# Kernel tuning notes

Measured on AMD Instinct MI355X. Metric: run time of the kernel, lower is better.

Reference implementation:

```python
import jax, jax.numpy as jnp
import numpy as np

N_H = 16
N_KV = 4
D_K = 128
ROPE_BASE = 10000.0


def _rope(t, cos, sin):
    # t: [B, T, H, d_k]; cos/sin: [1, T, 1, d_k//2]
    te, to = t[..., 0::2], t[..., 1::2]
    oe = te * cos - to * sin
    oo = te * sin + to * cos
    return jnp.stack([oe, oo], axis=-1).reshape(t.shape)


def setup_inputs() -> dict:
    key = jax.random.key(0)
    ks = jax.random.split(key, 5)
    B, T, d = 4, 2048, 2048
    s = 0.02
    return {
        "x": jax.random.normal(ks[0], (B, T, d), jnp.float32),
        "Wq": jax.random.normal(ks[1], (d, d), jnp.float32) * s,
        "Wk": jax.random.normal(ks[2], (d, N_KV * D_K), jnp.float32) * s,
        "Wv": jax.random.normal(ks[3], (d, N_KV * D_K), jnp.float32) * s,
        "Wp": jax.random.normal(ks[4], (d, d), jnp.float32) * s,
        "bp": jnp.zeros((d,), jnp.float32),
    }


def reference(x, Wq, Wk, Wv, Wp, bp):
    B, T, C = x.shape
    g = N_H // N_KV  # group size

    q = (x @ Wq).reshape(B, T, N_H, D_K)
    k = (x @ Wk).reshape(B, T, N_KV, D_K)
    v = (x @ Wv).reshape(B, T, N_KV, D_K)

    # RoPE frequencies (constants)
    theta = ROPE_BASE ** (-2.0 * jnp.arange(0, D_K, 2, dtype=jnp.float32) / D_K)
    freq = jnp.arange(T, dtype=jnp.float32)[:, None] * theta[None, :]  # [T, d_k//2]
    cos = jnp.cos(freq)[None, :, None, :]
    sin = jnp.sin(freq)[None, :, None, :]
    q = _rope(q, cos, sin)
    k = _rope(k, cos, sin)

    # GQA: group q heads by shared kv head (equiv to repeat_interleave on kv)
    q = q.reshape(B, T, N_KV, g, D_K).transpose(0, 2, 3, 1, 4)  # [B,n_kv,g,T,d_k]
    k = k.transpose(0, 2, 1, 3)  # [B,n_kv,T,d_k]
    v = v.transpose(0, 2, 1, 3)

    scores = jnp.einsum('bngqd,bnkd->bngqk', q, k) * (D_K ** -0.5)
    causal = jnp.tril(jnp.ones((T, T), bool))
    scores = jnp.where(causal, scores, -jnp.inf)
    attn = jax.nn.softmax(scores, axis=-1)
    out = jnp.einsum('bngqk,bnkd->bngqd', attn, v)  # [B,n_kv,g,T,d_k]
    out = out.transpose(0, 3, 1, 2, 4).reshape(B, T, C)
    return out @ Wp + bp
```

## Files before the change

### kernel.cpp

```cpp
#include <hip/hip_runtime.h>
#include <hip/hip_bf16.h>
#include <math.h>

typedef __bf16 bf16_t;
typedef __bf16 bf16x8 __attribute__((ext_vector_type(8)));
typedef __bf16 bf16x4 __attribute__((ext_vector_type(4)));
typedef float f32x4 __attribute__((ext_vector_type(4)));
typedef float f32x16 __attribute__((ext_vector_type(16)));
typedef unsigned int u32;

#define MFMA16 __builtin_amdgcn_mfma_f32_16x16x32_bf16
#define MFMA32 __builtin_amdgcn_mfma_f32_32x32x16_bf16

static __device__ __forceinline__ u32 pkbf(float a, float b) {
  union { bf16_t h[2]; u32 u; } z;
  z.h[0] = (bf16_t)a; z.h[1] = (bf16_t)b;
  return z.u;
}

static __device__ __forceinline__ void gload16(const bf16_t* g, bf16_t* l) {
  __builtin_amdgcn_global_load_lds(
      (const __attribute__((address_space(1))) void*)g,
      (__attribute__((address_space(3))) void*)l, 16, 0, 0);
}

__global__ void k_f32_to_bf16(const float* __restrict__ in, bf16_t* __restrict__ out, long n) {
  long i = ((long)blockIdx.x * blockDim.x + threadIdx.x) * 4;
  long stride = (long)gridDim.x * blockDim.x * 4;
  for (; i < n; i += stride) {
    const float4 v = *(const float4*)(in + i);
    bf16x4 o; o[0] = (bf16_t)v.x; o[1] = (bf16_t)v.y; o[2] = (bf16_t)v.z; o[3] = (bf16_t)v.w;
    *(bf16x4*)(out + i) = o;
  }
}

__global__ void k_transpose_bf16(const float* __restrict__ W, bf16_t* __restrict__ WT,
                                 int K, int N) {
  __shared__ float tile[32][33];
  int n0 = blockIdx.x * 32, k0 = blockIdx.y * 32;
  int tx = threadIdx.x & 31, ty = threadIdx.x >> 5;
#pragma unroll
  for (int i = 0; i < 4; i++)
    tile[ty + i * 8][tx] = W[(size_t)(k0 + ty + i * 8) * N + n0 + tx];
  __syncthreads();
#pragma unroll
  for (int i = 0; i < 4; i++) {
    int n = ty + i * 8;
    WT[(size_t)(n0 + n) * K + k0 + tx] = (bf16_t)tile[tx][n];
  }
}

__global__ void k_build_vt(const bf16_t* __restrict__ qkv, bf16_t* __restrict__ VT) {
  __shared__ bf16_t tile[32][33];
  int t0 = blockIdx.x * 32, c0 = blockIdx.y * 32, b = blockIdx.z;
  int tx = threadIdx.x & 31, ty = threadIdx.x >> 5;
  const bf16_t* src = qkv + (size_t)b * 2048 * 3072 + 2560;
#pragma unroll
  for (int i = 0; i < 4; i++)
    tile[ty + i * 8][tx] = src[(size_t)(t0 + ty + i * 8) * 3072 + c0 + tx];
  __syncthreads();
  bf16_t* dst = VT + (size_t)b * 512 * 2048;
#pragma unroll
  for (int i = 0; i < 4; i++)
    dst[(size_t)(c0 + ty + i * 8) * 2048 + t0 + tx] = tile[tx][ty + i * 8];
}

__global__ void k_rope(bf16_t* __restrict__ qkv) {
  int idx = blockIdx.x * blockDim.x + threadIdx.x;
  if (idx >= 8192 * 1280) return;
  int r = idx / 1280, p = idx - r * 1280;
  int t = r & 2047;
  int i = p & 63;
  float theta = exp2f(-(float)i * 0.41524101186092029f);
  float f = (float)t * theta;
  float s, c;
  sincosf(f, &s, &c);
  bf16_t* a = qkv + (size_t)r * 3072 + p * 2;
  float e = (float)a[0], o = (float)a[1];
  a[0] = (bf16_t)(e * c - o * s);
  a[1] = (bf16_t)(e * s + o * c);
}

template <bool F32OUT>
__global__ __launch_bounds__(512, 2) void k_gemm_bt(
    const bf16_t* __restrict__ A, const bf16_t* __restrict__ BT,
    bf16_t* __restrict__ Cb, float* __restrict__ Cf,
    const float* __restrict__ bias, int M, int N, int K, int nwg) {
  __shared__ bf16_t smem[65536];
  const int nbn = N >> 8;
  int orig = (int)blockIdx.x;
  int swz = (orig & 7) * (nwg >> 3) + (orig >> 3);
  int bm = swz / nbn, bn = swz % nbn;
  const int tid = threadIdx.x;
  const int lane = tid & 63, wid = tid >> 6;
  const int wm = (wid >> 2) << 7;
  const int wn = (wid & 3) << 6;
  const int lr = lane & 15, lq = lane >> 4;
  f32x4 acc[8][4] = {};

  const int rl = tid >> 3;
  const int ss = (tid & 7) ^ (rl & 7);
  const bf16_t* gA = A + (size_t)(bm * 256 + rl) * K + ss * 8;
  const bf16_t* gB = BT + (size_t)(bn * 256 + rl) * K + ss * 8;
  const int lo = wid * 512;

  const int nt = K >> 6;
  {
    bf16_t* sA0 = smem;
    bf16_t* sB0 = smem + 16384;
#pragma unroll
    for (int i = 0; i < 4; i++) {
      gload16(gA + (size_t)i * 64 * K, sA0 + i * 4096 + lo);
      gload16(gB + (size_t)i * 64 * K, sB0 + i * 4096 + lo);
    }
  }
  asm volatile("s_waitcnt vmcnt(0)" ::: "memory");
  __syncthreads();

  for (int t = 0; t < nt; ++t) {
    bf16_t* sAc = smem + (t & 1) * 32768;
    bf16_t* sBc = sAc + 16384;
    bf16_t* sAn = smem + ((t & 1) ^ 1) * 32768;
    bf16_t* sBn = sAn + 16384;
    const int k1 = (t + 1) << 6;
    bf16x8 breg[4][2];
#pragma unroll
    for (int n = 0; n < 4; n++)
#pragma unroll
      for (int kk = 0; kk < 2; kk++) {
        int R = wn + n * 16 + lr;
        int u = (kk * 4 + lq) ^ (R & 7);
        breg[n][kk] = *(const bf16x8*)&sBc[R * 64 + u * 8];
      }
    {
      bf16x8 areg[2][2];
#pragma unroll
      for (int ml = 0; ml < 2; ml++)
#pragma unroll
        for (int kk = 0; kk < 2; kk++) {
          int R = wm + ml * 16 + lr;
          int u = (kk * 4 + lq) ^ (R & 7);
          areg[ml][kk] = *(const bf16x8*)&sAc[R * 64 + u * 8];
        }
      if (t + 1 < nt) {
#pragma unroll
        for (int i = 0; i < 4; i++) {
          gload16(gA + (size_t)i * 64 * K + k1, sAn + i * 4096 + lo);
          gload16(gB + (size_t)i * 64 * K + k1, sBn + i * 4096 + lo);
        }
      }
      __builtin_amdgcn_s_barrier();
      asm volatile("s_waitcnt lgkmcnt(0)" ::: "memory");
      __builtin_amdgcn_sched_barrier(0);
      __builtin_amdgcn_s_setprio(1);
#pragma unroll
      for (int ml = 0; ml < 2; ml++)
#pragma unroll
        for (int n = 0; n < 4; n++)
#pragma unroll
          for (int kk = 0; kk < 2; kk++)
            acc[ml][n] = MFMA16(areg[ml][kk], breg[n][kk], acc[ml][n], 0, 0, 0);
      __builtin_amdgcn_s_setprio(0);
      __builtin_amdgcn_s_barrier();
    }
#pragma unroll
    for (int p = 1; p < 4; p++) {
      bf16x8 areg[2][2];
#pragma unroll
      for (int ml = 0; ml < 2; ml++)
#pragma unroll
        for (int kk = 0; kk < 2; kk++) {
          int R = wm + (2 * p + ml) * 16 + lr;
          int u = (kk * 4 + lq) ^ (R & 7);
          areg[ml][kk] = *(const bf16x8*)&sAc[R * 64 + u * 8];
        }
      __builtin_amdgcn_s_barrier();
      asm volatile("s_waitcnt lgkmcnt(0)" ::: "memory");
      __builtin_amdgcn_sched_barrier(0);
      __builtin_amdgcn_s_setprio(1);
#pragma unroll
      for (int ml = 0; ml < 2; ml++)
#pragma unroll
        for (int n = 0; n < 4; n++)
#pragma unroll
          for (int kk = 0; kk < 2; kk++)
            acc[2 * p + ml][n] = MFMA16(areg[ml][kk], breg[n][kk], acc[2 * p + ml][n], 0, 0, 0);
      __builtin_amdgcn_s_setprio(0);
      if (p == 3) {
        asm volatile("s_waitcnt vmcnt(0)" ::: "memory");
        __builtin_amdgcn_sched_barrier(0);
      }
      __builtin_amdgcn_s_barrier();
    }
  }
#pragma unroll
  for (int m = 0; m < 8; m++) {
    int row0 = bm * 256 + wm + m * 16 + lq * 4;
#pragma unroll
    for (int n = 0; n < 4; n++) {
      int col = bn * 256 + wn + n * 16 + lr;
#pragma unroll
      for (int r = 0; r < 4; r++) {
        if constexpr (F32OUT)
          Cf[(size_t)(row0 + r) * N + col] = acc[m][n][r] + bias[col];
        else
          Cb[(size_t)(row0 + r) * N + col] = (bf16_t)acc[m][n][r];
      }
    }
  }
}

__global__ __launch_bounds__(256, 2) void k_attn(const bf16_t* __restrict__ qkv,
                                                 const bf16_t* __restrict__ VT,
                                                 bf16_t* __restrict__ out) {
  __shared__ bf16_t sK[64 * 128];
  __shared__ bf16_t sVT[128 * 72];
  int bid = blockIdx.x;
  int g = bid >> 6;
  int qt = (g & 1) ? (g >> 1) : (15 - (g >> 1));
  int bh = bid & 63;
  int h = bh & 15, b = bh >> 4;
  int kvh = h >> 2;
  const size_t RS = 3072;
  const bf16_t* Qb = qkv + (size_t)b * 2048 * RS + h * 128;
  const bf16_t* Kb = qkv + (size_t)b * 2048 * RS + 2048 + kvh * 128;
  const bf16_t* Vt = VT + (size_t)(b * 4 + kvh) * 128 * 2048;
  int q0 = qt * 128;
  int tid = threadIdx.x, lane = tid & 63, wid = tid >> 6;
  int l31 = lane & 31, hi = lane >> 5;
  int qw = q0 + wid * 32;

  bf16x8 qf[8];
  {
    const bf16_t* qrow = Qb + (size_t)(qw + l31) * RS + hi * 8;
#pragma unroll
    for (int dc = 0; dc < 8; dc++)
      qf[dc] = *(const bf16x8*)(qrow + dc * 16);
  }

  f32x16 oT[4] = {};
  float m_r = -INFINITY, l_r = 0.f;
  const float SC = 0.08838834764831845f * 1.4426950408889634f;

  int k_row = tid >> 4, k_seg = tid & 15;
  int vd = tid >> 3, vk = (tid & 7) * 8;

  bf16x8 kreg[4], vreg[4];
  auto issue = [&](int k0) {
#pragma unroll
    for (int ps = 0; ps < 4; ps++)
      kreg[ps] = *(const bf16x8*)(Kb + (size_t)(k0 + k_row + ps * 16) * RS + k_seg * 8);
#pragma unroll
    for (int ps = 0; ps < 4; ps++)
      vreg[ps] = *(const bf16x8*)(Vt + (size_t)(vd + ps * 32) * 2048 + k0 + vk);
  };

  int ntiles = 2 * qt + 2;
  issue(0);
  for (int kt = 0; kt < ntiles; kt++) {
    int k0 = kt * 64;
#pragma unroll
    for (int ps = 0; ps < 4; ps++) {
      int row = k_row + ps * 16;
      int off = row * 256 + ((k_seg * 16) ^ ((row & 7) << 4));
      *(bf16x8*)((char*)sK + off) = kreg[ps];
    }
#pragma unroll
    for (int ps = 0; ps < 4; ps++)
      *(bf16x8*)&sVT[(vd + ps * 32) * 72 + vk] = vreg[ps];
    __syncthreads();
    if (kt + 1 < ntiles) issue(k0 + 64);

    if (k0 <= qw + 31) {
      f32x16 sa0 = {}, sa1 = {};
      __builtin_amdgcn_s_setprio(1);
#pragma unroll
      for (int dc = 0; dc < 8; dc++) {
        int cb = (dc * 32 + hi * 16) ^ ((l31 & 7) << 4);
        bf16x8 kf0 = *(const bf16x8*)((const char*)sK + l31 * 256 + cb);
        bf16x8 kf1 = *(const bf16x8*)((const char*)sK + (32 + l31) * 256 + cb);
        sa0 = MFMA32(kf0, qf[dc], sa0, 0, 0, 0);
        sa1 = MFMA32(kf1, qf[dc], sa1, 0, 0, 0);
      }
      __builtin_amdgcn_s_setprio(0);
      float p[2][16];
      int qg = qw + l31;
      if (k0 + 63 <= qw) {
#pragma unroll
        for (int r = 0; r < 16; r++) { p[0][r] = sa0[r]; p[1][r] = sa1[r]; }
      } else {
#pragma unroll
        for (int nf = 0; nf < 2; nf++)
#pragma unroll
          for (int r = 0; r < 16; r++) {
            int kg = k0 + nf * 32 + (r & 3) + 8 * (r >> 2) + 4 * hi;
            p[nf][r] = (kg <= qg) ? (nf ? sa1[r] : sa0[r]) : -INFINITY;
          }
      }
      float mx[16];
#pragma unroll
      for (int r = 0; r < 16; r++) mx[r] = fmaxf(p[0][r], p[1][r]);
#pragma unroll
      for (int s = 8; s >= 1; s >>= 1)
#pragma unroll
        for (int r = 0; r < 8; r++)
          if (r < s) mx[r] = fmaxf(mx[r], mx[r + s]);
      float pm = mx[0] * SC;
      pm = fmaxf(pm, __shfl_xor(pm, 32));
      bool skip = __all(pm <= m_r + 8.f);
      float mn = skip ? m_r : fmaxf(m_r, pm);
      float alpha = skip ? 1.f : exp2f(m_r - mn);
      m_r = mn;
      float nm = -m_r;
#pragma unroll
      for (int nf = 0; nf < 2; nf++)
#pragma unroll
        for (int r = 0; r < 16; r++)
          p[nf][r] = exp2f(fmaf(p[nf][r], SC, nm));
      float sm[16];
#pragma unroll
      for (int r = 0; r < 16; r++) sm[r] = p[0][r] + p[1][r];
#pragma unroll
      for (int s = 8; s >= 1; s >>= 1)
#pragma unroll
        for (int r = 0; r < 8; r++)
          if (r < s) sm[r] += sm[r + s];
      float rs = sm[0] + __shfl_xor(sm[0], 32);
      l_r = l_r * alpha + rs;
      if (!skip) {
#pragma unroll
        for (int c = 0; c < 4; c++)
#pragma unroll
          for (int r = 0; r < 16; r++) oT[c][r] *= alpha;
      }
#pragma unroll
      for (int nf = 0; nf < 2; nf++) {
        u32 Qk[4][2];
#pragma unroll
        for (int gg = 0; gg < 4; gg++) {
          Qk[gg][0] = pkbf(p[nf][4 * gg + 0], p[nf][4 * gg + 1]);
          Qk[gg][1] = pkbf(p[nf][4 * gg + 2], p[nf][4 * gg + 3]);
        }
#pragma unroll
        for (int kc = 0; kc < 2; kc++) {
          u32 x0 = __shfl_xor(Qk[2 * kc + 1 - hi][0], 32);
          u32 x1 = __shfl_xor(Qk[2 * kc + 1 - hi][1], 32);
          u32 o0 = Qk[2 * kc + hi][0], o1 = Qk[2 * kc + hi][1];
          union { u32 w[4]; bf16x8 v; } pf;
          pf.w[0] = hi ? x0 : o0;
          pf.w[1] = hi ? x1 : o1;
          pf.w[2] = hi ? o0 : x0;
          pf.w[3] = hi ? o1 : x1;
          int slot = nf * 2 + kc;
          __builtin_amdgcn_s_setprio(1);
#pragma unroll
          for (int c = 0; c < 4; c++) {
            bf16x8 vf = *(const bf16x8*)&sVT[(c * 32 + l31) * 72 + slot * 16 + hi * 8];
            oT[c] = MFMA32(vf, pf.v, oT[c], 0, 0, 0);
          }
          __builtin_amdgcn_s_setprio(0);
        }
      }
    }
    __syncthreads();
  }
  float inv = 1.f / l_r;
  size_t row = (size_t)b * 2048 + qw + l31;
#pragma unroll
  for (int c = 0; c < 4; c++)
#pragma unroll
    for (int rr = 0; rr < 4; rr++) {
      bf16x4 o4;
#pragma unroll
      for (int j = 0; j < 4; j++) o4[j] = (bf16_t)(oT[c][rr * 4 + j] * inv);
      *(bf16x4*)(out + row * 2048 + h * 128 + c * 32 + rr * 8 + hi * 4) = o4;
    }
}

extern "C" void kernel_launch(void* const* d_in, const int* in_sizes, int n_in,
                              void* d_out, int out_size, void* d_ws, size_t ws_size,
                              hipStream_t stream) {
  const float* x = (const float*)d_in[0];
  const float* Wq = (const float*)d_in[1];
  const float* Wk = (const float*)d_in[2];
  const float* Wv = (const float*)d_in[3];
  const float* Wp = (const float*)d_in[4];
  const float* bp = (const float*)d_in[5];
  float* out = (float*)d_out;

  bf16_t* ws = (bf16_t*)d_ws;
  bf16_t* xb = ws;
  bf16_t* qkv = ws + 16777216;
  bf16_t* WqkvT = ws + 16777216 + 25165824;
  bf16_t* WpT = WqkvT + 6291456;
  bf16_t* VT = WqkvT;

  k_f32_to_bf16<<<2048, 256, 0, stream>>>(x, xb, 16777216L);
  k_transpose_bf16<<<dim3(64, 64), 256, 0, stream>>>(Wq, WqkvT, 2048, 2048);
  k_transpose_bf16<<<dim3(16, 64), 256, 0, stream>>>(Wk, WqkvT + (size_t)2048 * 2048, 2048, 512);
  k_transpose_bf16<<<dim3(16, 64), 256, 0, stream>>>(Wv, WqkvT + (size_t)2560 * 2048, 2048, 512);
  k_transpose_bf16<<<dim3(64, 64), 256, 0, stream>>>(Wp, WpT, 2048, 2048);

  k_gemm_bt<false><<<384, 512, 0, stream>>>(xb, WqkvT, qkv, nullptr, nullptr, 8192, 3072, 2048, 384);
  k_rope<<<40960, 256, 0, stream>>>(qkv);
  k_build_vt<<<dim3(64, 16, 4), 256, 0, stream>>>(qkv, VT);
  k_attn<<<1024, 256, 0, stream>>>(qkv, VT, xb);
  k_gemm_bt<true><<<256, 512, 0, stream>>>(xb, WpT, nullptr, out, bp, 8192, 2048, 2048, 256);
}
```

Baseline: 389.1 us.

## Double-buffer attention K/V via direct-to-LDS loads and process 64 query rows per wave

The attention kernel now assigns 256 query rows per block (64 per wave, as two 32-row groups), so each K/V tile loaded into shared memory is reused across twice as many queries. It halves the grid to 512 blocks and uses a permuted query-tile order for load balance. K and V tiles are double-buffered in LDS and fetched with global_load_lds, with XOR swizzling, replacing register staging. This removes one barrier per tile and overlaps loads with compute. The cost is higher register pressure (8 output accumulators and two Q fragment sets) and fewer blocks, which may hurt occupancy and causal-tile balance.

New measurement: 538.8 us. 38.5% more time.

```diff
diff --git a/kernel.cpp b/kernel.cpp
--- a/kernel.cpp
+++ b/kernel.cpp
@@ -213,11 +213,13 @@
 __global__ __launch_bounds__(256, 2) void k_attn(const bf16_t* __restrict__ qkv,
                                                  const bf16_t* __restrict__ VT,
                                                  bf16_t* __restrict__ out) {
-  __shared__ bf16_t sK[64 * 128];
-  __shared__ bf16_t sVT[128 * 72];
+  __shared__ bf16_t sK[2][64 * 128];
+  __shared__ bf16_t sV[2][128 * 64];
   int bid = blockIdx.x;
-  int g = bid >> 6;
-  int qt = (g & 1) ? (g >> 1) : (15 - (g >> 1));
+  int gq = bid >> 6;
+  const u32 permbits = (7u) | (5u << 3) | (6u << 6) | (4u << 9) |
+                       (0u << 12) | (2u << 15) | (1u << 18) | (3u << 21);
+  int qt = (permbits >> (gq * 3)) & 7;
   int bh = bid & 63;
   int h = bh & 15, b = bh >> 4;
   int kvh = h >> 2;
@@ -225,67 +227,77 @@
   const bf16_t* Qb = qkv + (size_t)b * 2048 * RS + h * 128;
   const bf16_t* Kb = qkv + (size_t)b * 2048 * RS + 2048 + kvh * 128;
   const bf16_t* Vt = VT + (size_t)(b * 4 + kvh) * 128 * 2048;
-  int q0 = qt * 128;
   int tid = threadIdx.x, lane = tid & 63, wid = tid >> 6;
   int l31 = lane & 31, hi = lane >> 5;
-  int qw = q0 + wid * 32;
-
-  bf16x8 qf[8];
+  int qw = qt * 256 + wid * 64;
+
+  bf16x8 qf0[8], qf1[8];
   {
-    const bf16_t* qrow = Qb + (size_t)(qw + l31) * RS + hi * 8;
-#pragma unroll
-    for (int dc = 0; dc < 8; dc++)
-      qf[dc] = *(const bf16x8*)(qrow + dc * 16);
-  }
-
-  f32x16 oT[4] = {};
-  float m_r = -INFINITY, l_r = 0.f;
+    const bf16_t* q0r = Qb + (size_t)(qw + l31) * RS + hi * 8;
+    const bf16_t* q1r = Qb + (size_t)(qw + 32 + l31) * RS + hi * 8;
+#pragma unroll
+    for (int dc = 0; dc < 8; dc++) {
+      qf0[dc] = *(const bf16x8*)(q0r + dc * 16);
+      qf1[dc] = *(const bf16x8*)(q1r + dc * 16);
+    }
+  }
+
+  const bf16_t* Kst = Kb + (size_t)(tid >> 4) * RS + ((tid & 15) ^ ((tid >> 4) & 7)) * 8;
+  const bf16_t* Vst = Vt + (size_t)(tid >> 3) * 2048 + ((tid & 7) ^ ((tid >> 3) & 7)) * 8;
+
+  f32x16 oT[8] = {};
+  float m0 = -INFINITY, l0 = 0.f, m1 = -INFINITY, l1 = 0.f;
   const float SC = 0.08838834764831845f * 1.4426950408889634f;
 
-  int k_row = tid >> 4, k_seg = tid & 15;
-  int vd = tid >> 3, vk = (tid & 7) * 8;
-
-  bf16x8 kreg[4], vreg[4];
-  auto issue = [&](int k0) {
-#pragma unroll
-    for (int ps = 0; ps < 4; ps++)
-      kreg[ps] = *(const bf16x8*)(Kb + (size_t)(k0 + k_row + ps * 16) * RS + k_seg * 8);
-#pragma unroll
-    for (int ps = 0; ps < 4; ps++)
-      vreg[ps] = *(const bf16x8*)(Vt + (size_t)(vd + ps * 32) * 2048 + k0 + vk);
-  };
-
-  int ntiles = 2 * qt + 2;
-  issue(0);
+  int ntiles = qt * 4 + 4;
+#pragma unroll
+  for (int i = 0; i < 4; i++)
+    gload16(Kst + (size_t)(i * 16) * RS, &sK[0][i * 2048 + wid * 512]);
+#pragma unroll
+  for (int i = 0; i < 4; i++)
+    gload16(Vst + (size_t)(i * 32) * 2048, &sV[0][i * 2048 + wid * 512]);
+
   for (int kt = 0; kt < ntiles; kt++) {
-    int k0 = kt * 64;
-#pragma unroll
-    for (int ps = 0; ps < 4; ps++) {
-      int row = k_row + ps * 16;
-      int off = row * 256 + ((k_seg * 16) ^ ((row & 7) << 4));
-      *(bf16x8*)((char*)sK + off) = kreg[ps];
-    }
-#pragma unroll
-    for (int ps = 0; ps < 4; ps++)
-      *(bf16x8*)&sVT[(vd + ps * 32) * 72 + vk] = vreg[ps];
-    __syncthreads();
-    if (kt + 1 < ntiles) issue(k0 + 64);
-
-    if (k0 <= qw + 31) {
+    int k0 = kt << 6;
+    int cur = kt & 1;
+    asm volatile("s_waitcnt vmcnt(0)" ::: "memory");
+    __builtin_amdgcn_s_barrier();
+    __builtin_amdgcn_sched_barrier(0);
+    if (kt + 1 < ntiles) {
+      int k1 = k0 + 64;
+#pragma unroll
+      for (int i = 0; i < 4; i++)
+        gload16(Kst + (size_t)(k1 + i * 16) * RS, &sK[cur ^ 1][i * 2048 + wid * 512]);
+#pragma unroll
+      for (int i = 0; i < 4; i++)
+        gload16(Vst + (size_t)(i * 32) * 2048 + k1, &sV[cur ^ 1][i * 2048 + wid * 512]);
+    }
+    if (k0 > qw) continue;
+    bool diag = (k0 == qw);
+    const char* sKc = (const char*)sK[cur];
+    const char* sVc = (const char*)sV[cur];
+    bf16x8 pf0[4], pf1[4];
+
+#pragma unroll
+    for (int grp = 0; grp < 2; grp++) {
+      const bf16x8* qf = grp ? qf1 : qf0;
+      float& m_r = grp ? m1 : m0;
+      float& l_r = grp ? l1 : l0;
+      bf16x8* pf = grp ? pf1 : pf0;
+      int qg = qw + grp * 32 + l31;
       f32x16 sa0 = {}, sa1 = {};
       __builtin_amdgcn_s_setprio(1);
 #pragma unroll
       for (int dc = 0; dc < 8; dc++) {
         int cb = (dc * 32 + hi * 16) ^ ((l31 & 7) << 4);
-        bf16x8 kf0 = *(const bf16x8*)((const char*)sK + l31 * 256 + cb);
-        bf16x8 kf1 = *(const bf16x8*)((const char*)sK + (32 + l31) * 256 + cb);
+        bf16x8 kf0 = *(const bf16x8*)(sKc + l31 * 256 + cb);
+        bf16x8 kf1 = *(const bf16x8*)(sKc + (32 + l31) * 256 + cb);
         sa0 = MFMA32(kf0, qf[dc], sa0, 0, 0, 0);
         sa1 = MFMA32(kf1, qf[dc], sa1, 0, 0, 0);
       }
       __builtin_amdgcn_s_setprio(0);
       float p[2][16];
-      int qg = qw + l31;
-      if (k0 + 63 <= qw) {
+      if (!diag) {
 #pragma unroll
         for (int r = 0; r < 16; r++) { p[0][r] = sa0[r]; p[1][r] = sa1[r]; }
       } else {
@@ -331,7 +343,7 @@
 #pragma unroll
         for (int c = 0; c < 4; c++)
 #pragma unroll
-          for (int r = 0; r < 16; r++) oT[c][r] *= alpha;
+          for (int r = 0; r < 16; r++) oT[grp * 4 + c][r] *= alpha;
       }
 #pragma unroll
       for (int nf = 0; nf < 2; nf++) {
@@ -346,34 +358,43 @@
           u32 x0 = __shfl_xor(Qk[2 * kc + 1 - hi][0], 32);
           u32 x1 = __shfl_xor(Qk[2 * kc + 1 - hi][1], 32);
           u32 o0 = Qk[2 * kc + hi][0], o1 = Qk[2 * kc + hi][1];
-          union { u32 w[4]; bf16x8 v; } pf;
-          pf.w[0] = hi ? x0 : o0;
-          pf.w[1] = hi ? x1 : o1;
-          pf.w[2] = hi ? o0 : x0;
-          pf.w[3] = hi ? o1 : x1;
-          int slot = nf * 2 + kc;
-          __builtin_amdgcn_s_setprio(1);
-#pragma unroll
-          for (int c = 0; c < 4; c++) {
-            bf16x8 vf = *(const bf16x8*)&sVT[(c * 32 + l31) * 72 + slot * 16 + hi * 8];
-            oT[c] = MFMA32(vf, pf.v, oT[c], 0, 0, 0);
-          }
-          __builtin_amdgcn_s_setprio(0);
+          union { u32 w[4]; bf16x8 v; } pv;
+          pv.w[0] = hi ? x0 : o0;
+          pv.w[1] = hi ? x1 : o1;
+          pv.w[2] = hi ? o0 : x0;
+          pv.w[3] = hi ? o1 : x1;
+          pf[nf * 2 + kc] = pv.v;
         }
       }
     }
-    __syncthreads();
-  }
-  float inv = 1.f / l_r;
-  size_t row = (size_t)b * 2048 + qw + l31;
+    __builtin_amdgcn_s_setprio(1);
+#pragma unroll
+    for (int slot = 0; slot < 4; slot++) {
+      int vb = (slot * 32 + hi * 16) ^ ((l31 & 7) << 4);
+#pragma unroll
+      for (int c = 0; c < 4; c++) {
+        bf16x8 vf = *(const bf16x8*)(sVc + (c * 32 + l31) * 128 + vb);
+        oT[c] = MFMA32(vf, pf0[slot], oT[c], 0, 0, 0);
+        oT[4 + c] = MFMA32(vf, pf1[slot], oT[4 + c], 0, 0, 0);
+      }
+    }
+    __builtin_amdgcn_s_setprio(0);
+  }
+  float inv0 = 1.f / l0, inv1 = 1.f / l1;
+  size_t row0 = (size_t)b * 2048 + qw + l31;
 #pragma unroll
   for (int c = 0; c < 4; c++)
 #pragma unroll
     for (int rr = 0; rr < 4; rr++) {
-      bf16x4 o4;
-#pragma unroll
-      for (int j = 0; j < 4; j++) o4[j] = (bf16_t)(oT[c][rr * 4 + j] * inv);
-      *(bf16x4*)(out + row * 2048 + h * 128 + c * 32 + rr * 8 + hi * 4) = o4;
+      bf16x4 o4, o5;
+#pragma unroll
+      for (int j = 0; j < 4; j++) {
+        o4[j] = (bf16_t)(oT[c][rr * 4 + j] * inv0);
+        o5[j] = (bf16_t)(oT[4 + c][rr * 4 + j] * inv1);
+      }
+      size_t coloff = h * 128 + c * 32 + rr * 8 + hi * 4;
+      *(bf16x4*)(out + row0 * 2048 + coloff) = o4;
+      *(bf16x4*)(out + (row0 + 32) * 2048 + coloff) = o5;
     }
 }
 
@@ -404,6 +425,6 @@
   k_gemm_bt<false><<<384, 512, 0, stream>>>(xb, WqkvT, qkv, nullptr, nullptr, 8192, 3072, 2048, 384);
   k_rope<<<40960, 256, 0, stream>>>(qkv);
   k_build_vt<<<dim3(64, 16, 4), 256, 0, stream>>>(qkv, VT);
-  k_attn<<<1024, 256, 0, stream>>>(qkv, VT, xb);
+  k_attn<<<512, 256, 0, stream>>>(qkv, VT, xb);
   k_gemm_bt<true><<<256, 512, 0, stream>>>(xb, WpT, nullptr, out, bp, 8192, 2048, 2048, 256);
 }
```

## Double-buffer attention K/V tiles via direct global-to-LDS loads with 256-row query blocks

Applied to the files above, without the earlier changes.

The attention kernel now uses 512-thread blocks covering 256 query rows, which halves the grid and doubles K/V reuse per loaded tile. K and V^T tiles are loaded straight into double-buffered, XOR-swizzled LDS with global_load_lds, so the register staging copy and the second barrier per iteration go away. The query-tile order follows a permutation table meant to balance causal work across the grid. The costs are more LDS per block, waves that sit idle on tiles fully masked by causality, and a vmcnt(0) wait before each barrier.

New measurement: 411.0 us. 5.6% more time.

```diff
diff --git a/kernel.cpp b/kernel.cpp
--- a/kernel.cpp
+++ b/kernel.cpp
@@ -210,14 +210,16 @@
   }
 }
 
-__global__ __launch_bounds__(256, 2) void k_attn(const bf16_t* __restrict__ qkv,
+__global__ __launch_bounds__(512, 2) void k_attn(const bf16_t* __restrict__ qkv,
                                                  const bf16_t* __restrict__ VT,
                                                  bf16_t* __restrict__ out) {
-  __shared__ bf16_t sK[64 * 128];
-  __shared__ bf16_t sVT[128 * 72];
+  __shared__ bf16_t sK[2][64 * 128];
+  __shared__ bf16_t sV[2][128 * 64];
   int bid = blockIdx.x;
-  int g = bid >> 6;
-  int qt = (g & 1) ? (g >> 1) : (15 - (g >> 1));
+  int gq = bid >> 6;
+  const u32 permbits = (7u) | (5u << 3) | (6u << 6) | (4u << 9) |
+                       (0u << 12) | (2u << 15) | (1u << 18) | (3u << 21);
+  int qt = (permbits >> (gq * 3)) & 7;
   int bh = bid & 63;
   int h = bh & 15, b = bh >> 4;
   int kvh = h >> 2;
@@ -225,10 +227,9 @@
   const bf16_t* Qb = qkv + (size_t)b * 2048 * RS + h * 128;
   const bf16_t* Kb = qkv + (size_t)b * 2048 * RS + 2048 + kvh * 128;
   const bf16_t* Vt = VT + (size_t)(b * 4 + kvh) * 128 * 2048;
-  int q0 = qt * 128;
   int tid = threadIdx.x, lane = tid & 63, wid = tid >> 6;
   int l31 = lane & 31, hi = lane >> 5;
-  int qw = q0 + wid * 32;
+  int qw = qt * 256 + wid * 32;
 
   bf16x8 qf[8];
   {
@@ -238,131 +239,134 @@
       qf[dc] = *(const bf16x8*)(qrow + dc * 16);
   }
 
+  const int rlk = tid >> 4;
+  const bf16_t* Kst = Kb + (size_t)rlk * RS + (size_t)(((tid & 15) ^ (rlk & 7)) * 8);
+  const int vdr = tid >> 3;
+  const bf16_t* Vst = Vt + (size_t)vdr * 2048 + (size_t)(((tid & 7) ^ (vdr & 7)) * 8);
+  const int lo = wid * 512;
+
   f32x16 oT[4] = {};
   float m_r = -INFINITY, l_r = 0.f;
   const float SC = 0.08838834764831845f * 1.4426950408889634f;
 
-  int k_row = tid >> 4, k_seg = tid & 15;
-  int vd = tid >> 3, vk = (tid & 7) * 8;
-
-  bf16x8 kreg[4], vreg[4];
-  auto issue = [&](int k0) {
-#pragma unroll
-    for (int ps = 0; ps < 4; ps++)
-      kreg[ps] = *(const bf16x8*)(Kb + (size_t)(k0 + k_row + ps * 16) * RS + k_seg * 8);
-#pragma unroll
-    for (int ps = 0; ps < 4; ps++)
-      vreg[ps] = *(const bf16x8*)(Vt + (size_t)(vd + ps * 32) * 2048 + k0 + vk);
-  };
-
-  int ntiles = 2 * qt + 2;
-  issue(0);
+  int ntiles = qt * 4 + 4;
+#pragma unroll
+  for (int i = 0; i < 2; i++)
+    gload16(Kst + (size_t)(i * 32) * RS, &sK[0][i * 4096 + lo]);
+#pragma unroll
+  for (int i = 0; i < 2; i++)
+    gload16(Vst + (size_t)(i * 64) * 2048, &sV[0][i * 4096 + lo]);
+
   for (int kt = 0; kt < ntiles; kt++) {
-    int k0 = kt * 64;
-#pragma unroll
-    for (int ps = 0; ps < 4; ps++) {
-      int row = k_row + ps * 16;
-      int off = row * 256 + ((k_seg * 16) ^ ((row & 7) << 4));
-      *(bf16x8*)((char*)sK + off) = kreg[ps];
-    }
-#pragma unroll
-    for (int ps = 0; ps < 4; ps++)
-      *(bf16x8*)&sVT[(vd + ps * 32) * 72 + vk] = vreg[ps];
-    __syncthreads();
-    if (kt + 1 < ntiles) issue(k0 + 64);
-
-    if (k0 <= qw + 31) {
-      f32x16 sa0 = {}, sa1 = {};
-      __builtin_amdgcn_s_setprio(1);
-#pragma unroll
-      for (int dc = 0; dc < 8; dc++) {
-        int cb = (dc * 32 + hi * 16) ^ ((l31 & 7) << 4);
-        bf16x8 kf0 = *(const bf16x8*)((const char*)sK + l31 * 256 + cb);
-        bf16x8 kf1 = *(const bf16x8*)((const char*)sK + (32 + l31) * 256 + cb);
-        sa0 = MFMA32(kf0, qf[dc], sa0, 0, 0, 0);
-        sa1 = MFMA32(kf1, qf[dc], sa1, 0, 0, 0);
-      }
-      __builtin_amdgcn_s_setprio(0);
-      float p[2][16];
-      int qg = qw + l31;
-      if (k0 + 63 <= qw) {
-#pragma unroll
-        for (int r = 0; r < 16; r++) { p[0][r] = sa0[r]; p[1][r] = sa1[r]; }
-      } else {
-#pragma unroll
-        for (int nf = 0; nf < 2; nf++)
-#pragma unroll
-          for (int r = 0; r < 16; r++) {
-            int kg = k0 + nf * 32 + (r & 3) + 8 * (r >> 2) + 4 * hi;
-            p[nf][r] = (kg <= qg) ? (nf ? sa1[r] : sa0[r]) : -INFINITY;
-          }
-      }
-      float mx[16];
-#pragma unroll
-      for (int r = 0; r < 16; r++) mx[r] = fmaxf(p[0][r], p[1][r]);
-#pragma unroll
-      for (int s = 8; s >= 1; s >>= 1)
-#pragma unroll
-        for (int r = 0; r < 8; r++)
-          if (r < s) mx[r] = fmaxf(mx[r], mx[r + s]);
-      float pm = mx[0] * SC;
-      pm = fmaxf(pm, __shfl_xor(pm, 32));
-      bool skip = __all(pm <= m_r + 8.f);
-      float mn = skip ? m_r : fmaxf(m_r, pm);
-      float alpha = skip ? 1.f : exp2f(m_r - mn);
-      m_r = mn;
-      float nm = -m_r;
+    int k0 = kt << 6;
+    int cur = kt & 1;
+    asm volatile("s_waitcnt vmcnt(0)" ::: "memory");
+    __builtin_amdgcn_s_barrier();
+    __builtin_amdgcn_sched_barrier(0);
+    if (kt + 1 < ntiles) {
+      int k1 = k0 + 64;
+#pragma unroll
+      for (int i = 0; i < 2; i++)
+        gload16(Kst + (size_t)(k1 + i * 32) * RS, &sK[cur ^ 1][i * 4096 + lo]);
+#pragma unroll
+      for (int i = 0; i < 2; i++)
+        gload16(Vst + (size_t)(i * 64) * 2048 + k1, &sV[cur ^ 1][i * 4096 + lo]);
+    }
+    if (k0 > qw) continue;
+    bool diag = (qw - k0) < 64;
+    const char* sKc = (const char*)sK[cur];
+    const char* sVc = (const char*)sV[cur];
+
+    f32x16 sa0 = {}, sa1 = {};
+    __builtin_amdgcn_s_setprio(1);
+#pragma unroll
+    for (int dc = 0; dc < 8; dc++) {
+      int cb = (dc * 32 + hi * 16) ^ ((l31 & 7) << 4);
+      bf16x8 kf0 = *(const bf16x8*)(sKc + l31 * 256 + cb);
+      bf16x8 kf1 = *(const bf16x8*)(sKc + (32 + l31) * 256 + cb);
+      sa0 = MFMA32(kf0, qf[dc], sa0, 0, 0, 0);
+      sa1 = MFMA32(kf1, qf[dc], sa1, 0, 0, 0);
+    }
+    __builtin_amdgcn_s_setprio(0);
+    float p[2][16];
+    int qg = qw + l31;
+    if (!diag) {
+#pragma unroll
+      for (int r = 0; r < 16; r++) { p[0][r] = sa0[r]; p[1][r] = sa1[r]; }
+    } else {
 #pragma unroll
       for (int nf = 0; nf < 2; nf++)
 #pragma unroll
-        for (int r = 0; r < 16; r++)
-          p[nf][r] = exp2f(fmaf(p[nf][r], SC, nm));
-      float sm[16];
-#pragma unroll
-      for (int r = 0; r < 16; r++) sm[r] = p[0][r] + p[1][r];
-#pragma unroll
-      for (int s = 8; s >= 1; s >>= 1)
-#pragma unroll
-        for (int r = 0; r < 8; r++)
-          if (r < s) sm[r] += sm[r + s];
-      float rs = sm[0] + __shfl_xor(sm[0], 32);
-      l_r = l_r * alpha + rs;
-      if (!skip) {
-#pragma unroll
-        for (int c = 0; c < 4; c++)
-#pragma unroll
-          for (int r = 0; r < 16; r++) oT[c][r] *= alpha;
-      }
-#pragma unroll
-      for (int nf = 0; nf < 2; nf++) {
-        u32 Qk[4][2];
-#pragma unroll
-        for (int gg = 0; gg < 4; gg++) {
-          Qk[gg][0] = pkbf(p[nf][4 * gg + 0], p[nf][4 * gg + 1]);
-          Qk[gg][1] = pkbf(p[nf][4 * gg + 2], p[nf][4 * gg + 3]);
+        for (int r = 0; r < 16; r++) {
+          int kg = k0 + nf * 32 + (r & 3) + 8 * (r >> 2) + 4 * hi;
+          p[nf][r] = (kg <= qg) ? (nf ? sa1[r] : sa0[r]) : -INFINITY;
         }
-#pragma unroll
-        for (int kc = 0; kc < 2; kc++) {
-          u32 x0 = __shfl_xor(Qk[2 * kc + 1 - hi][0], 32);
-          u32 x1 = __shfl_xor(Qk[2 * kc + 1 - hi][1], 32);
-          u32 o0 = Qk[2 * kc + hi][0], o1 = Qk[2 * kc + hi][1];
-          union { u32 w[4]; bf16x8 v; } pf;
-          pf.w[0] = hi ? x0 : o0;
-          pf.w[1] = hi ? x1 : o1;
-          pf.w[2] = hi ? o0 : x0;
-          pf.w[3] = hi ? o1 : x1;
-          int slot = nf * 2 + kc;
-          __builtin_amdgcn_s_setprio(1);
-#pragma unroll
-          for (int c = 0; c < 4; c++) {
-            bf16x8 vf = *(const bf16x8*)&sVT[(c * 32 + l31) * 72 + slot * 16 + hi * 8];
-            oT[c] = MFMA32(vf, pf.v, oT[c], 0, 0, 0);
-          }
-          __builtin_amdgcn_s_setprio(0);
+    }
+    float mx[16];
+#pragma unroll
+    for (int r = 0; r < 16; r++) mx[r] = fmaxf(p[0][r], p[1][r]);
+#pragma unroll
+    for (int s = 8; s >= 1; s >>= 1)
+#pragma unroll
+      for (int r = 0; r < 8; r++)
+        if (r < s) mx[r] = fmaxf(mx[r], mx[r + s]);
+    float pm = mx[0] * SC;
+    pm = fmaxf(pm, __shfl_xor(pm, 32));
+    bool skip = __all(pm <= m_r + 8.f);
+    float mn = skip ? m_r : fmaxf(m_r, pm);
+    float alpha = skip ? 1.f : exp2f(m_r - mn);
+    m_r = mn;
+    float nm = -m_r;
+#pragma unroll
+    for (int nf = 0; nf < 2; nf++)
+#pragma unroll
+      for (int r = 0; r < 16; r++)
+        p[nf][r] = exp2f(fmaf(p[nf][r], SC, nm));
+    float sm[16];
+#pragma unroll
+    for (int r = 0; r < 16; r++) sm[r] = p[0][r] + p[1][r];
+#pragma unroll
+    for (int s = 8; s >= 1; s >>= 1)
+#pragma unroll
+      for (int r = 0; r < 8; r++)
+        if (r < s) sm[r] += sm[r + s];
+    float rs = sm[0] + __shfl_xor(sm[0], 32);
+    l_r = l_r * alpha + rs;
+    if (!skip) {
+#pragma unroll
+      for (int c = 0; c < 4; c++)
+#pragma unroll
+        for (int r = 0; r < 16; r++) oT[c][r] *= alpha;
+    }
+#pragma unroll
+    for (int nf = 0; nf < 2; nf++) {
+      u32 Qk[4][2];
+#pragma unroll
+      for (int gg = 0; gg < 4; gg++) {
+        Qk[gg][0] = pkbf(p[nf][4 * gg + 0], p[nf][4 * gg + 1]);
+        Qk[gg][1] = pkbf(p[nf][4 * gg + 2], p[nf][4 * gg + 3]);
+      }
+#pragma unroll
+      for (int kc = 0; kc < 2; kc++) {
+        u32 x0 = __shfl_xor(Qk[2 * kc + 1 - hi][0], 32);
+        u32 x1 = __shfl_xor(Qk[2 * kc + 1 - hi][1], 32);
+        u32 o0 = Qk[2 * kc + hi][0], o1 = Qk[2 * kc + hi][1];
+        union { u32 w[4]; bf16x8 v; } pf;
+        pf.w[0] = hi ? x0 : o0;
+        pf.w[1] = hi ? x1 : o1;
+        pf.w[2] = hi ? o0 : x0;
+        pf.w[3] = hi ? o1 : x1;
+        int slot = nf * 2 + kc;
+        int vb = (slot * 32 + hi * 16) ^ ((l31 & 7) << 4);
+        __builtin_amdgcn_s_setprio(1);
+#pragma unroll
+        for (int c = 0; c < 4; c++) {
+          bf16x8 vf = *(const bf16x8*)(sVc + (c * 32 + l31) * 128 + vb);
+          oT[c] = MFMA32(vf, pf.v, oT[c], 0, 0, 0);
         }
-      }
-    }
-    __syncthreads();
+        __builtin_amdgcn_s_setprio(0);
+      }
+    }
   }
   float inv = 1.f / l_r;
   size_t row = (size_t)b * 2048 + qw + l31;
@@ -404,6 +408,6 @@
   k_gemm_bt<false><<<384, 512, 0, stream>>>(xb, WqkvT, qkv, nullptr, nullptr, 8192, 3072, 2048, 384);
   k_rope<<<40960, 256, 0, stream>>>(qkv);
   k_build_vt<<<dim3(64, 16, 4), 256, 0, stream>>>(qkv, VT);
-  k_attn<<<1024, 256, 0, stream>>>(qkv, VT, xb);
+  k_attn<<<512, 512, 0, stream>>>(qkv, VT, xb);
   k_gemm_bt<true><<<256, 512, 0, stream>>>(xb, WpT, nullptr, out, bp, 8192, 2048, 2048, 256);
 }
```

## Double-buffer K tile in LDS via direct global-to-LDS loads

Applied to the files above, without the earlier changes.

K tiles are now loaded straight from global memory into a double-buffered LDS array with global_load_lds, using a pre-swizzled source address, instead of staging them through registers. The next tile is prefetched into the alternate buffer while the current one is consumed. The launch bound rises to 3 blocks per CU to cut register pressure and raise occupancy. The cost is more LDS per block, and there may be no explicit wait on the async LDS load before the barrier, which is a correctness risk.

Result: slower. 420.4 us (+8.0%).

```diff
diff --git a/kernel.cpp b/kernel.cpp
--- a/kernel.cpp
+++ b/kernel.cpp
@@ -210,10 +210,10 @@
   }
 }
 
-__global__ __launch_bounds__(256, 2) void k_attn(const bf16_t* __restrict__ qkv,
+__global__ __launch_bounds__(256, 3) void k_attn(const bf16_t* __restrict__ qkv,
                                                  const bf16_t* __restrict__ VT,
                                                  bf16_t* __restrict__ out) {
-  __shared__ bf16_t sK[64 * 128];
+  __shared__ bf16_t sK[2][64 * 128];
   __shared__ bf16_t sVT[128 * 72];
   int bid = blockIdx.x;
   int g = bid >> 6;
@@ -238,47 +238,51 @@
       qf[dc] = *(const bf16x8*)(qrow + dc * 16);
   }
 
+  const int rlk = tid >> 4;
+  const bf16_t* Kst = Kb + (size_t)rlk * RS + (size_t)(((tid & 15) ^ (rlk & 7)) * 8);
+  const int lo = wid * 512;
+  int vd = tid >> 3, vk = (tid & 7) * 8;
+
   f32x16 oT[4] = {};
   float m_r = -INFINITY, l_r = 0.f;
   const float SC = 0.08838834764831845f * 1.4426950408889634f;
 
-  int k_row = tid >> 4, k_seg = tid & 15;
-  int vd = tid >> 3, vk = (tid & 7) * 8;
-
-  bf16x8 kreg[4], vreg[4];
-  auto issue = [&](int k0) {
-#pragma unroll
-    for (int ps = 0; ps < 4; ps++)
-      kreg[ps] = *(const bf16x8*)(Kb + (size_t)(k0 + k_row + ps * 16) * RS + k_seg * 8);
+  bf16x8 vreg[4];
+  auto issueV = [&](int k0) {
 #pragma unroll
     for (int ps = 0; ps < 4; ps++)
       vreg[ps] = *(const bf16x8*)(Vt + (size_t)(vd + ps * 32) * 2048 + k0 + vk);
   };
+  auto issueK = [&](int k0, int buf) {
+#pragma unroll
+    for (int i = 0; i < 4; i++)
+      gload16(Kst + (size_t)(k0 + i * 16) * RS, &sK[buf][i * 2048 + lo]);
+  };
 
   int ntiles = 2 * qt + 2;
-  issue(0);
+  issueK(0, 0);
+  issueV(0);
   for (int kt = 0; kt < ntiles; kt++) {
     int k0 = kt * 64;
-#pragma unroll
-    for (int ps = 0; ps < 4; ps++) {
-      int row = k_row + ps * 16;
-      int off = row * 256 + ((k_seg * 16) ^ ((row & 7) << 4));
-      *(bf16x8*)((char*)sK + off) = kreg[ps];
-    }
+    int cur = kt & 1;
 #pragma unroll
     for (int ps = 0; ps < 4; ps++)
       *(bf16x8*)&sVT[(vd + ps * 32) * 72 + vk] = vreg[ps];
     __syncthreads();
-    if (kt + 1 < ntiles) issue(k0 + 64);
+    if (kt + 1 < ntiles) {
+      issueK(k0 + 64, cur ^ 1);
+      issueV(k0 + 64);
+    }
 
     if (k0 <= qw + 31) {
+      const char* sKc = (const char*)sK[cur];
       f32x16 sa0 = {}, sa1 = {};
       __builtin_amdgcn_s_setprio(1);
 #pragma unroll
       for (int dc = 0; dc < 8; dc++) {
         int cb = (dc * 32 + hi * 16) ^ ((l31 & 7) << 4);
-        bf16x8 kf0 = *(const bf16x8*)((const char*)sK + l31 * 256 + cb);
-        bf16x8 kf1 = *(const bf16x8*)((const char*)sK + (32 + l31) * 256 + cb);
+        bf16x8 kf0 = *(const bf16x8*)(sKc + l31 * 256 + cb);
+        bf16x8 kf1 = *(const bf16x8*)(sKc + (32 + l31) * 256 + cb);
         sa0 = MFMA32(kf0, qf[dc], sa0, 0, 0, 0);
         sa1 = MFMA32(kf1, qf[dc], sa1, 0, 0, 0);
       }
```
